# Kernel tuning notes

Measured on AMD Instinct MI355X. Metric: run time of the kernel, lower is better.

The kernel has to match this reference:

```python
import jax, jax.numpy as jnp
import numpy as np

B, H, W, C = 32, 224, 224, 3
HID = 64


def setup_inputs() -> dict:
    key = jax.random.key(0)
    k0, k1, k2 = jax.random.split(key, 3)
    inputs = jax.random.normal(k0, (B, H, W, C), dtype=jnp.float32)
    # Localization-net dense params. Original uses zeros init (identity transform);
    # we use small random weights plus the identity affine bias so the sampling
    # grid is a nontrivial perturbation of identity.
    w1 = jax.random.normal(k1, (H * W * C, HID), dtype=jnp.float32) * 1e-3
    b1 = jnp.zeros((HID,), dtype=jnp.float32)
    w2 = jax.random.normal(k2, (HID, 6), dtype=jnp.float32) * 1e-2
    b2 = jnp.array([1.0, 0.0, 0.0, 0.0, 1.0, 0.0], dtype=jnp.float32)
    return {"inputs": inputs, "w1": w1, "b1": b1, "w2": w2, "b2": b2}


def _bilinear_sampler(img, x_s, y_s):
    # img: [B,H,W,C]; x_s, y_s: [B,H,W] normalized coords in [-1,1]
    Bn, Hn, Wn, Cn = img.shape
    x = 0.5 * (x_s + 1.0) * (Wn - 1)
    y = 0.5 * (y_s + 1.0) * (Hn - 1)
    x0 = jnp.floor(x).astype(jnp.int32)
    x1 = x0 + 1
    y0 = jnp.floor(y).astype(jnp.int32)
    y1 = y0 + 1
    x0c = jnp.clip(x0, 0, Wn - 1)
    x1c = jnp.clip(x1, 0, Wn - 1)
    y0c = jnp.clip(y0, 0, Hn - 1)
    y1c = jnp.clip(y1, 0, Hn - 1)
    b_idx = jnp.arange(Bn, dtype=jnp.int32)[:, None, None]
    Ia = img[b_idx, y0c, x0c]  # [B,H,W,C]
    Ib = img[b_idx, y1c, x0c]
    Ic = img[b_idx, y0c, x1c]
    Id = img[b_idx, y1c, x1c]
    x0f = x0c.astype(x.dtype)
    x1f = x1c.astype(x.dtype)
    y0f = y0c.astype(y.dtype)
    y1f = y1c.astype(y.dtype)
    wa = ((x1f - x) * (y1f - y))[..., None]
    wb = ((x1f - x) * (y - y0f))[..., None]
    wc = ((x - x0f) * (y1f - y))[..., None]
    wd = ((x - x0f) * (y - y0f))[..., None]
    return wa * Ia + wb * Ib + wc * Ic + wd * Id


def reference(inputs, w1, b1, w2, b2):
    Bn, Hn, Wn, Cn = inputs.shape
    # NOTE: original keras code overwrites the conv branch with flatten(inputs),
    # so the conv/maxpool layers are dead code and omitted. Dropout is identity
    # at inference (training=False).
    flat = inputs.reshape(Bn, -1)
    h = jnp.tanh(flat @ w1 + b1)
    theta = jnp.tanh(h @ w2 + b2).reshape(Bn, 2, 3)
    # affine sampling grid over normalized target coords
    xt, yt = jnp.meshgrid(
        jnp.linspace(-1.0, 1.0, Wn, dtype=inputs.dtype),
        jnp.linspace(-1.0, 1.0, Hn, dtype=inputs.dtype),
    )  # each [H,W]
    grid = jnp.stack([xt.ravel(), yt.ravel(), jnp.ones_like(xt).ravel()])  # [3,H*W]
    batch_grid = jnp.einsum("bij,jk->bik", theta, grid).reshape(Bn, 2, Hn, Wn)
    x_s = batch_grid[:, 0]
    y_s = batch_grid[:, 1]
    return _bilinear_sampler(inputs, x_s, y_s)
```

## Files before the change

kernel.cpp:

```cpp
#include <hip/hip_runtime.h>

#define BATCH 32
#define HDIM 224
#define WDIM 224
#define CDIM 3
#define KTOT (HDIM * WDIM * CDIM)
#define HID 64
#define KCHUNK 128
#define NBLK1 (KTOT / KCHUNK)
#define PIX (HDIM * WDIM)
#define BLK3 49

__global__ __launch_bounds__(256, 5) void k1_gemm(const float* __restrict__ flat,
                                                  const float* __restrict__ w1,
                                                  float* __restrict__ hacc) {
    __shared__ float smem[6144];
    const int tid  = threadIdx.x;
    const int lane = tid & 63;
    const int wave = tid >> 6;
    const int k0   = blockIdx.x * KCHUNK;
    const int kw   = wave * 32;

    float w[32];
    const float* wp = w1 + (size_t)(k0 + kw) * HID + lane;
#pragma unroll
    for (int i = 0; i < 32; ++i)
        w[i] = wp[(size_t)i * HID];

#pragma unroll
    for (int t = 0; t < 4; ++t) {
        const int idx = tid + t * 256;
        const int b   = idx >> 5;
        const int kq  = idx & 31;
        *(float4*)(smem + idx * 4) =
            *(const float4*)(flat + (size_t)b * KTOT + k0 + kq * 4);
    }
    __syncthreads();

    float acc[32];
#pragma unroll
    for (int j = 0; j < 32; ++j) acc[j] = 0.0f;

#pragma unroll
    for (int kk = 0; kk < 32; kk += 4) {
#pragma unroll
        for (int b = 0; b < 32; ++b) {
            const float4 x = *(const float4*)(smem + b * 128 + kw + kk);
            float a = acc[b];
            a = fmaf(x.x, w[kk + 0], a);
            a = fmaf(x.y, w[kk + 1], a);
            a = fmaf(x.z, w[kk + 2], a);
            a = fmaf(x.w, w[kk + 3], a);
            acc[b] = a;
        }
    }
    __syncthreads();

    if (wave) {
#pragma unroll
        for (int j = 0; j < 32; ++j)
            smem[(wave - 1) * 2048 + j * 64 + lane] = acc[j];
    }
    __syncthreads();
    if (wave == 0) {
#pragma unroll
        for (int j = 0; j < 32; ++j) {
            const int idx = j * 64 + lane;
            atomicAdd(hacc + idx,
                      acc[j] + smem[idx] + smem[2048 + idx] + smem[4096 + idx]);
        }
    }
}

__global__ __launch_bounds__(256) void k3_sample(const float* __restrict__ img,
                                                 const float* __restrict__ hacc,
                                                 const float* __restrict__ b1,
                                                 const float* __restrict__ w2,
                                                 const float* __restrict__ b2,
                                                 float* __restrict__ out) {
    const int b     = blockIdx.x / BLK3;
    const int strip = blockIdx.x - b * BLK3;
    const int tid   = threadIdx.x;

    __shared__ float sh[HID];
    __shared__ float sth[6];
    if (tid < HID)
        sh[tid] = tanhf(hacc[b * HID + tid] + b1[tid]);
    __syncthreads();
    if (tid < 6) {
        float s = b2[tid];
#pragma unroll
        for (int t = 0; t < HID; ++t)
            s = fmaf(sh[t], w2[t * 6 + tid], s);
        sth[tid] = tanhf(s);
    }
    __syncthreads();

    const float t0 = sth[0], t1 = sth[1], t2 = sth[2];
    const float t3 = sth[3], t4 = sth[4], t5 = sth[5];

    const float* base = img + (size_t)b * KTOT;
    const int pix0 = strip * 1024 + tid * 4;

    float res[12];
#pragma unroll
    for (int p = 0; p < 4; ++p) {
        const int pix = pix0 + p;
        const int i = pix / WDIM;
        const int j = pix - i * WDIM;

        const float xt = (2.0f * (float)j - (float)(WDIM - 1)) / (float)(WDIM - 1);
        const float yt = (2.0f * (float)i - (float)(HDIM - 1)) / (float)(HDIM - 1);

        const float xs = t0 * xt + t1 * yt + t2;
        const float ys = t3 * xt + t4 * yt + t5;

        const float x = 0.5f * (xs + 1.0f) * (float)(WDIM - 1);
        const float y = 0.5f * (ys + 1.0f) * (float)(HDIM - 1);

        const int x0 = (int)floorf(x);
        const int y0 = (int)floorf(y);

        const int x0c = min(max(x0, 0), WDIM - 1);
        const int x1c = min(max(x0 + 1, 0), WDIM - 1);
        const int y0c = min(max(y0, 0), HDIM - 1);
        const int y1c = min(max(y0 + 1, 0), HDIM - 1);

        const float x0f = (float)x0c, x1f = (float)x1c;
        const float y0f = (float)y0c, y1f = (float)y1c;

        const float wa = (x1f - x) * (y1f - y);
        const float wb = (x1f - x) * (y - y0f);
        const float wc = (x - x0f) * (y1f - y);
        const float wd = (x - x0f) * (y - y0f);

        const float* pa = base + (size_t)(y0c * WDIM + x0c) * 3;
        const float* pb = base + (size_t)(y1c * WDIM + x0c) * 3;
        const float* pc = base + (size_t)(y0c * WDIM + x1c) * 3;
        const float* pd = base + (size_t)(y1c * WDIM + x1c) * 3;

#pragma unroll
        for (int c = 0; c < 3; ++c)
            res[p * 3 + c] = wa * pa[c] + wb * pb[c] + wc * pc[c] + wd * pd[c];
    }

    float4* po = (float4*)(out + (size_t)b * KTOT + (size_t)pix0 * 3);
    po[0] = make_float4(res[0], res[1], res[2],  res[3]);
    po[1] = make_float4(res[4], res[5], res[6],  res[7]);
    po[2] = make_float4(res[8], res[9], res[10], res[11]);
}

extern "C" void kernel_launch(void* const* d_in, const int* in_sizes, int n_in,
                              void* d_out, int out_size, void* d_ws, size_t ws_size,
                              hipStream_t stream) {
    const float* inputs = (const float*)d_in[0];
    const float* w1     = (const float*)d_in[1];
    const float* b1     = (const float*)d_in[2];
    const float* w2     = (const float*)d_in[3];
    const float* b2     = (const float*)d_in[4];
    float* out = (float*)d_out;

    float* hacc = (float*)d_ws;

    hipMemsetAsync(hacc, 0, BATCH * HID * sizeof(float), stream);
    k1_gemm<<<NBLK1, 256, 0, stream>>>(inputs, w1, hacc);
    k3_sample<<<BATCH * BLK3, 256, 0, stream>>>(inputs, hacc, b1, w2, b2, out);
}
```

Before: 141.4 us.

## Replace atomic split-K accumulation with partial buffer and separate reduce kernel

Doubles the K chunk per GEMM block, which halves the block count. Each block now writes its full 32x64 partial result to a workspace buffer instead of issuing atomicAdds into the accumulator. A new reduction kernel sums the partials across blocks, and the memset is no longer needed. This removes atomic contention and the memset launch, at the cost of an extra kernel, extra global traffic for the partials, and more registers per thread (occupancy hint lowered to 4).

```diff
diff --git a/kernel.cpp b/kernel.cpp
--- a/kernel.cpp
+++ b/kernel.cpp
@@ -6,33 +6,33 @@
 #define CDIM 3
 #define KTOT (HDIM * WDIM * CDIM)
 #define HID 64
-#define KCHUNK 128
+#define KCHUNK 256
 #define NBLK1 (KTOT / KCHUNK)
 #define PIX (HDIM * WDIM)
 #define BLK3 49
 
-__global__ __launch_bounds__(256, 5) void k1_gemm(const float* __restrict__ flat,
+__global__ __launch_bounds__(256, 4) void k1_gemm(const float* __restrict__ flat,
                                                   const float* __restrict__ w1,
-                                                  float* __restrict__ hacc) {
-    __shared__ float smem[6144];
+                                                  float* __restrict__ part) {
+    __shared__ float smem[8192];
     const int tid  = threadIdx.x;
     const int lane = tid & 63;
     const int wave = tid >> 6;
     const int k0   = blockIdx.x * KCHUNK;
-    const int kw   = wave * 32;
+    const int kw   = wave * 64;
 
-    float w[32];
+    float w[64];
     const float* wp = w1 + (size_t)(k0 + kw) * HID + lane;
 #pragma unroll
-    for (int i = 0; i < 32; ++i)
+    for (int i = 0; i < 64; ++i)
         w[i] = wp[(size_t)i * HID];
 
 #pragma unroll
-    for (int t = 0; t < 4; ++t) {
+    for (int t = 0; t < 8; ++t) {
         const int idx = tid + t * 256;
-        const int b   = idx >> 5;
-        const int kq  = idx & 31;
-        *(float4*)(smem + idx * 4) =
+        const int b   = idx >> 6;
+        const int kq  = idx & 63;
+        *(float4*)(smem + b * 256 + kq * 4) =
             *(const float4*)(flat + (size_t)b * KTOT + k0 + kq * 4);
     }
     __syncthreads();
@@ -42,10 +42,10 @@
     for (int j = 0; j < 32; ++j) acc[j] = 0.0f;
 
 #pragma unroll
-    for (int kk = 0; kk < 32; kk += 4) {
+    for (int kk = 0; kk < 64; kk += 4) {
 #pragma unroll
         for (int b = 0; b < 32; ++b) {
-            const float4 x = *(const float4*)(smem + b * 128 + kw + kk);
+            const float4 x = *(const float4*)(smem + b * 256 + kw + kk);
             float a = acc[b];
             a = fmaf(x.x, w[kk + 0], a);
             a = fmaf(x.y, w[kk + 1], a);
@@ -56,19 +56,39 @@
     }
     __syncthreads();
 
-    if (wave) {
 #pragma unroll
-        for (int j = 0; j < 32; ++j)
-            smem[(wave - 1) * 2048 + j * 64 + lane] = acc[j];
+    for (int j = 0; j < 32; ++j)
+        smem[wave * 2048 + j * 64 + lane] = acc[j];
+    __syncthreads();
+
+    float* po = part + (size_t)blockIdx.x * 2048;
+#pragma unroll
+    for (int t = 0; t < 8; ++t) {
+        const int idx = tid + t * 256;
+        po[idx] = smem[idx] + smem[2048 + idx] +
+                  smem[4096 + idx] + smem[6144 + idx];
     }
+}
+
+__global__ __launch_bounds__(256) void k1_reduce(const float* __restrict__ part,
+                                                 float* __restrict__ hacc) {
+    __shared__ float red[256];
+    const int tid    = threadIdx.x;
+    const int o      = tid & 31;
+    const int g      = tid >> 5;
+    const int o_base = blockIdx.x * 32;
+
+    float s = 0.0f;
+    for (int blk = g; blk < NBLK1; blk += 8)
+        s += part[(size_t)blk * 2048 + o_base + o];
+    red[tid] = s;
     __syncthreads();
-    if (wave == 0) {
+    if (g == 0) {
+        float t = 0.0f;
 #pragma unroll
-        for (int j = 0; j < 32; ++j) {
-            const int idx = j * 64 + lane;
-            atomicAdd(hacc + idx,
-                      acc[j] + smem[idx] + smem[2048 + idx] + smem[4096 + idx]);
-        }
+        for (int gg = 0; gg < 8; ++gg)
+            t += red[gg * 32 + o];
+        hacc[o_base + o] = t;
     }
 }
 
@@ -160,9 +180,10 @@
     const float* b2     = (const float*)d_in[4];
     float* out = (float*)d_out;
 
-    float* hacc = (float*)d_ws;
+    float* part = (float*)d_ws;
+    float* hacc = part + (size_t)NBLK1 * 2048;
 
-    hipMemsetAsync(hacc, 0, BATCH * HID * sizeof(float), stream);
-    k1_gemm<<<NBLK1, 256, 0, stream>>>(inputs, w1, hacc);
+    k1_gemm<<<NBLK1, 256, 0, stream>>>(inputs, w1, part);
+    k1_reduce<<<HID * BATCH / 32, 256, 0, stream>>>(part, hacc);
     k3_sample<<<BATCH * BLK3, 256, 0, stream>>>(inputs, hacc, b1, w2, b2, out);
 }
```

Result: slower. 152.1 us (+7.6%).

## Stage w1 chunk in LDS and broadcast inputs via uniform loads in GEMM

Applied to the files above, without the earlier changes.

The localization GEMM kernel is reorganised. Each block now stages its 128x64 slice of w1 in shared memory. Each wave owns 8 batch rows across the whole K chunk, reading input values with wave-uniform addresses (readfirstlane), which lets them be served as broadcast or scalar loads. This removes the cross-wave shared-memory reduction and a pair of barriers. The trade-offs are 32KB of LDS per block, which may limit occupancy, and loads of the input rows that are no longer coalesced.

```diff
diff --git a/kernel.cpp b/kernel.cpp
--- a/kernel.cpp
+++ b/kernel.cpp
@@ -6,70 +6,50 @@
 #define CDIM 3
 #define KTOT (HDIM * WDIM * CDIM)
 #define HID 64
-#define KCHUNK 128
-#define NBLK1 (KTOT / KCHUNK)
+#define KC 128
+#define NBLK1 (KTOT / KC)
 #define PIX (HDIM * WDIM)
 #define BLK3 49
 
 __global__ __launch_bounds__(256, 5) void k1_gemm(const float* __restrict__ flat,
                                                   const float* __restrict__ w1,
                                                   float* __restrict__ hacc) {
-    __shared__ float smem[6144];
+    __shared__ float sw[KC * HID];
     const int tid  = threadIdx.x;
     const int lane = tid & 63;
-    const int wave = tid >> 6;
-    const int k0   = blockIdx.x * KCHUNK;
-    const int kw   = wave * 32;
+    const int b0   = __builtin_amdgcn_readfirstlane((tid >> 6) * 8);
+    const int k0   = blockIdx.x * KC;
 
-    float w[32];
-    const float* wp = w1 + (size_t)(k0 + kw) * HID + lane;
+    const float4* wsrc = (const float4*)(w1 + (size_t)k0 * HID);
 #pragma unroll
-    for (int i = 0; i < 32; ++i)
-        w[i] = wp[(size_t)i * HID];
-
-#pragma unroll
-    for (int t = 0; t < 4; ++t) {
+    for (int t = 0; t < 8; ++t) {
         const int idx = tid + t * 256;
-        const int b   = idx >> 5;
-        const int kq  = idx & 31;
-        *(float4*)(smem + idx * 4) =
-            *(const float4*)(flat + (size_t)b * KTOT + k0 + kq * 4);
+        *(float4*)(sw + idx * 4) = wsrc[idx];
     }
     __syncthreads();
 
-    float acc[32];
+    float acc[8];
 #pragma unroll
-    for (int j = 0; j < 32; ++j) acc[j] = 0.0f;
+    for (int j = 0; j < 8; ++j) acc[j] = 0.0f;
+
+#pragma unroll 4
+    for (int kk = 0; kk < KC; kk += 4) {
+        float4 xs[8];
+#pragma unroll
+        for (int j = 0; j < 8; ++j)
+            xs[j] = *(const float4*)(flat + (size_t)(b0 + j) * KTOT + k0 + kk);
+#pragma unroll
+        for (int i = 0; i < 4; ++i) {
+            const float wv = sw[(kk + i) * HID + lane];
+#pragma unroll
+            for (int j = 0; j < 8; ++j)
+                acc[j] = fmaf(((const float*)&xs[j])[i], wv, acc[j]);
+        }
+    }
 
 #pragma unroll
-    for (int kk = 0; kk < 32; kk += 4) {
-#pragma unroll
-        for (int b = 0; b < 32; ++b) {
-            const float4 x = *(const float4*)(smem + b * 128 + kw + kk);
-            float a = acc[b];
-            a = fmaf(x.x, w[kk + 0], a);
-            a = fmaf(x.y, w[kk + 1], a);
-            a = fmaf(x.z, w[kk + 2], a);
-            a = fmaf(x.w, w[kk + 3], a);
-            acc[b] = a;
-        }
-    }
-    __syncthreads();
-
-    if (wave) {
-#pragma unroll
-        for (int j = 0; j < 32; ++j)
-            smem[(wave - 1) * 2048 + j * 64 + lane] = acc[j];
-    }
-    __syncthreads();
-    if (wave == 0) {
-#pragma unroll
-        for (int j = 0; j < 32; ++j) {
-            const int idx = j * 64 + lane;
-            atomicAdd(hacc + idx,
-                      acc[j] + smem[idx] + smem[2048 + idx] + smem[4096 + idx]);
-        }
-    }
+    for (int j = 0; j < 8; ++j)
+        atomicAdd(hacc + (b0 + j) * HID + lane, acc[j]);
 }
 
 __global__ __launch_bounds__(256) void k3_sample(const float* __restrict__ img,
```

Measured after the change: 165.7 us. +17.2%, slower.
